# Kernel optimization log

Measured on AMD Instinct MI355X. Metric: run time of the kernel, lower is better.

Reference implementation:

```python
import jax, jax.numpy as jnp
import numpy as np

T, B, H = 2048, 32, 1024
L1, L2, L3 = 100, 10, 1  # cascade 100 -> 10 -> 1 from linear_size=100


def setup_inputs() -> dict:
    key = jax.random.key(0)
    ks = jax.random.split(key, 8)
    def lin_init(k, fan_in, shape):
        # torch nn.Linear default: U(-1/sqrt(fan_in), 1/sqrt(fan_in))
        bound = 1.0 / np.sqrt(fan_in)
        return jax.random.uniform(k, shape, jnp.float32, -bound, bound)
    return {
        "encoder_output": jax.random.normal(ks[0], (T, B, H), jnp.float32),
        "lengths": jax.random.randint(ks[1], (B,), 1, T + 1, jnp.int64),
        "W1": lin_init(ks[2], H, (L1, H)),
        "b1": lin_init(ks[3], H, (L1,)),
        "W2": lin_init(ks[4], L1, (L2, L1)),
        "b2": lin_init(ks[5], L1, (L2,)),
        "W3": lin_init(ks[6], L2, (L3, L2)),
        "b3": lin_init(ks[7], L2, (L3,)),
    }


def reference(encoder_output, lengths, W1, b1, W2, b2, W3, b3):
    # MLP cascade over all timesteps/batch at once: [T,B,H] -> [T,B,1]
    h = jax.nn.relu(jnp.einsum("tbh,lh->tbl", encoder_output, W1) + b1)
    h = jax.nn.relu(jnp.einsum("tbl,ml->tbm", h, W2) + b2)
    logits = jnp.einsum("tbm,om->tbo", h, W3) + b3  # [T,B,1]
    logp = jax.nn.log_sigmoid(logits)[..., 0]       # [T,B]
    # Mask timesteps beyond each sample's length, sum, exponentiate
    mask = jnp.arange(T)[:, None] < lengths[None, :]  # [T,B]
    return jnp.exp(jnp.sum(jnp.where(mask, logp, 0.0), axis=0))  # [B]
```

## Files before the change

### kernel.cpp

```cpp
#include <hip/hip_runtime.h>
#include <stdint.h>


#define T_DIM 2048
#define B_DIM 32
#define H_DIM 1024
#define L1_DIM 100
#define L1_PAD 112
#define L2_DIM 10
#define L2_PAD 16
#define K2_PAD 128
#define NBLK  1024

#define W1B_ELEMS (L1_PAD * H_DIM)
#define W2B_ELEMS (L2_PAD * K2_PAD)
#define PART_OFF_BYTES ((W1B_ELEMS + W2B_ELEMS) * 2)

typedef float v4f __attribute__((ext_vector_type(4)));
typedef short s8  __attribute__((ext_vector_type(8)));

static __device__ __forceinline__ unsigned short f2bf(float f) {
    unsigned int u = __float_as_uint(f);
    u += 0x7fffu + ((u >> 16) & 1u);
    return (unsigned short)(u >> 16);
}

__global__ void convert_weights(const float* __restrict__ W1,
                                const float* __restrict__ W2,
                                unsigned short* __restrict__ wsb) {
    int i = blockIdx.x * 256 + threadIdx.x;
    if (i < W1B_ELEMS) {
        int row = i >> 10, col = i & 1023;
        float v = (row < L1_DIM) ? W1[row * H_DIM + col] : 0.0f;
        wsb[i] = f2bf(v);
    } else {
        int j = i - W1B_ELEMS;
        if (j < W2B_ELEMS) {
            int r = j >> 7, c = j & 127;
            float v = (r < L2_DIM && c < L1_DIM) ? W2[r * L1_DIM + c] : 0.0f;
            wsb[W1B_ELEMS + j] = f2bf(v);
        }
    }
}

__global__ __launch_bounds__(256) void mlp_main(
    const float* __restrict__ enc,
    const int*   __restrict__ lenp,
    const float* __restrict__ b1,
    const float* __restrict__ b2,
    const float* __restrict__ W3,
    const float* __restrict__ b3,
    const unsigned short* __restrict__ w1b,
    const unsigned short* __restrict__ w2b,
    float* __restrict__ partials)
{
    __shared__ __align__(16) unsigned short ldsB[L1_PAD][72];
    __shared__ __align__(16) unsigned short ldsH[64][136];
    __shared__ __align__(16) unsigned short ldsW2[L2_PAD][136];
    __shared__ float ldsPart[2][32];

    const int tid  = threadIdx.x;
    const int blk  = blockIdx.x;
    const int lane = tid & 63;
    const int w    = tid >> 6;
    const int m    = lane & 15;
    const int q    = lane >> 4;

    const bool is64 = (lenp[1] == 0);

    const int tA = 2 * blk + (w >> 1);
    const int bA = ((w & 1) << 4) + m;
    const int lenA = is64 ? lenp[2 * bA] : lenp[bA];
    const bool predA = (tA < lenA);

    int maxlen = 0;
    for (int i = 0; i < B_DIM; ++i) {
        int L = is64 ? lenp[2 * i] : lenp[i];
        maxlen = max(maxlen, L);
    }
    if (2 * blk >= maxlen) {
        if (tid < 32) partials[tid * NBLK + blk] = 0.0f;
        return;
    }

    {
        int r = tid >> 4;
        int c = (tid & 15) << 3;
        *(uint4*)&ldsW2[r][c] = *(const uint4*)(w2b + r * K2_PAD + c);
    }

    float b1v[7];
#pragma unroll
    for (int nt = 0; nt < 7; ++nt) {
        int n = nt * 16 + m;
        b1v[nt] = (n < L1_DIM) ? b1[n] : 0.0f;
    }
    const float b2v = (m < L2_DIM) ? b2[m] : 0.0f;
    const float w3v = (m < L2_DIM) ? W3[m] : 0.0f;
    const float b3s = b3[0];

    const float* aptr = enc + (size_t)(blk * 64 + w * 16 + m) * H_DIM + q * 8;

    v4f acc[7];
#pragma unroll
    for (int nt = 0; nt < 7; ++nt) acc[nt] = (v4f)0.0f;

    for (int kc = 0; kc < 16; ++kc) {
        __syncthreads();
        {
            int base = tid;
#pragma unroll
            for (int it = 0; it < 4; ++it, base += 256) {
                if (it < 3 || base < 896) {
                    int r = base >> 3;
                    int c = (base & 7) << 3;
                    *(uint4*)&ldsB[r][c] =
                        *(const uint4*)(w1b + r * H_DIM + kc * 64 + c);
                }
            }
        }
        __syncthreads();
#pragma unroll
        for (int ks = 0; ks < 2; ++ks) {
            const int k0 = kc * 64 + ks * 32;
            float4 x0, x1;
            if (predA) {
                x0 = *(const float4*)(aptr + k0);
                x1 = *(const float4*)(aptr + k0 + 4);
            } else {
                x0 = make_float4(0.f, 0.f, 0.f, 0.f);
                x1 = make_float4(0.f, 0.f, 0.f, 0.f);
            }
            s8 afrag;
            afrag[0] = (short)f2bf(x0.x); afrag[1] = (short)f2bf(x0.y);
            afrag[2] = (short)f2bf(x0.z); afrag[3] = (short)f2bf(x0.w);
            afrag[4] = (short)f2bf(x1.x); afrag[5] = (short)f2bf(x1.y);
            afrag[6] = (short)f2bf(x1.z); afrag[7] = (short)f2bf(x1.w);
#pragma unroll
            for (int nt = 0; nt < 7; ++nt) {
                s8 bfrag = *(const s8*)&ldsB[nt * 16 + m][ks * 32 + q * 8];
                acc[nt] = __builtin_amdgcn_mfma_f32_16x16x32_bf16(
                    afrag, bfrag, acc[nt], 0, 0, 0);
            }
        }
    }

    __syncthreads();
#pragma unroll
    for (int nt = 0; nt < 7; ++nt) {
#pragma unroll
        for (int reg = 0; reg < 4; ++reg) {
            float h = fmaxf(acc[nt][reg] + b1v[nt], 0.0f);
            ldsH[w * 16 + q * 4 + reg][nt * 16 + m] = f2bf(h);
        }
    }
    {
        int r = tid >> 2;
        int c = 112 + ((tid & 3) << 2);
        *(uint2*)&ldsH[r][c] = make_uint2(0u, 0u);
    }
    __syncthreads();

    v4f acc2 = (v4f)0.0f;
#pragma unroll
    for (int ks = 0; ks < 4; ++ks) {
        s8 a2  = *(const s8*)&ldsH[w * 16 + m][ks * 32 + q * 8];
        s8 b2f = *(const s8*)&ldsW2[m][ks * 32 + q * 8];
        acc2 = __builtin_amdgcn_mfma_f32_16x16x32_bf16(a2, b2f, acc2, 0, 0, 0);
    }

    v4f z;
#pragma unroll
    for (int reg = 0; reg < 4; ++reg) {
        float y2 = fmaxf(acc2[reg] + b2v, 0.0f);
        z[reg] = y2 * w3v;
    }
#pragma unroll
    for (int msk = 1; msk < 16; msk <<= 1) {
#pragma unroll
        for (int reg = 0; reg < 4; ++reg)
            z[reg] += __shfl_xor(z[reg], msk, 16);
    }
    if (m == 0) {
#pragma unroll
        for (int reg = 0; reg < 4; ++reg) {
            int rowLocal = q * 4 + reg;
            int bC = ((w & 1) << 4) + rowLocal;
            int lenC = is64 ? lenp[2 * bC] : lenp[bC];
            float logit = z[reg] + b3s;
            float logp  = fminf(logit, 0.0f) - log1pf(__expf(-fabsf(logit)));
            ldsPart[w >> 1][bC] = (tA < lenC) ? logp : 0.0f;
        }
    }
    __syncthreads();
    if (tid < 32)
        partials[tid * NBLK + blk] = ldsPart[0][tid] + ldsPart[1][tid];
}

__global__ void finalize(const float* __restrict__ partials,
                         float* __restrict__ out) {
    const int b = blockIdx.x;
    const int tid = threadIdx.x;
    float s = 0.0f;
    for (int i = tid; i < NBLK; i += 256) s += partials[b * NBLK + i];
#pragma unroll
    for (int off = 32; off > 0; off >>= 1) s += __shfl_down(s, off, 64);
    __shared__ float red[4];
    if ((tid & 63) == 0) red[tid >> 6] = s;
    __syncthreads();
    if (tid == 0) out[b] = expf(red[0] + red[1] + red[2] + red[3]);
}

extern "C" void kernel_launch(void* const* d_in, const int* in_sizes, int n_in,
                              void* d_out, int out_size, void* d_ws, size_t ws_size,
                              hipStream_t stream) {
    const float* enc = (const float*)d_in[0];
    const int*   len = (const int*)d_in[1];
    const float* W1  = (const float*)d_in[2];
    const float* b1  = (const float*)d_in[3];
    const float* W2  = (const float*)d_in[4];
    const float* b2  = (const float*)d_in[5];
    const float* W3  = (const float*)d_in[6];
    const float* b3  = (const float*)d_in[7];

    unsigned short* wsb = (unsigned short*)d_ws;
    float* partials = (float*)((char*)d_ws + PART_OFF_BYTES);
    float* out = (float*)d_out;

    convert_weights<<<(W1B_ELEMS + W2B_ELEMS + 255) / 256, 256, 0, stream>>>(W1, W2, wsb);
    mlp_main<<<NBLK, 256, 0, stream>>>(enc, len, b1, b2, W3, b3,
                                       wsb, wsb + W1B_ELEMS, partials);
    finalize<<<B_DIM, 256, 0, stream>>>(partials, out);
}
```

Measured before the change: 374.5 us.

## Double-buffer W1 tiles via direct-to-LDS loads and strided timestep slots

Moves to 512-thread blocks that each cover four timesteps spaced TSLOT apart, so work stays balanced under length masking. W1 tiles now go into a double-buffered, XOR-swizzled LDS buffer through global_load_lds, and the next encoder chunk is prefetched into registers so loads overlap the MFMA work. Waves whose rows are all masked skip the MFMAs. The second layer reads W2 straight from global memory, and H uses a swizzled layout to avoid bank conflicts. The early-exit on max length is removed, and the larger block needs more registers and LDS per block.

```diff
diff --git a/kernel.cpp b/kernel.cpp
--- a/kernel.cpp
+++ b/kernel.cpp
@@ -10,7 +10,8 @@
 #define L2_DIM 10
 #define L2_PAD 16
 #define K2_PAD 128
-#define NBLK  1024
+#define NBLK  512
+#define TSLOT 512
 
 #define W1B_ELEMS (L1_PAD * H_DIM)
 #define W2B_ELEMS (L2_PAD * K2_PAD)
@@ -43,7 +44,7 @@
     }
 }
 
-__global__ __launch_bounds__(256) void mlp_main(
+__global__ __launch_bounds__(512, 4) void mlp_main(
     const float* __restrict__ enc,
     const int*   __restrict__ lenp,
     const float* __restrict__ b1,
@@ -54,10 +55,9 @@
     const unsigned short* __restrict__ w2b,
     float* __restrict__ partials)
 {
-    __shared__ __align__(16) unsigned short ldsB[L1_PAD][72];
-    __shared__ __align__(16) unsigned short ldsH[64][136];
-    __shared__ __align__(16) unsigned short ldsW2[L2_PAD][136];
-    __shared__ float ldsPart[2][32];
+    __shared__ __align__(16) unsigned short bufB[2][L1_PAD * 64];
+    __shared__ __align__(16) unsigned short ldsH[128 * 128];
+    __shared__ float ldsPart[4][32];
 
     const int tid  = threadIdx.x;
     const int blk  = blockIdx.x;
@@ -65,29 +65,16 @@
     const int w    = tid >> 6;
     const int m    = lane & 15;
     const int q    = lane >> 4;
+    const int mx   = m & 7;
 
     const bool is64 = (lenp[1] == 0);
 
-    const int tA = 2 * blk + (w >> 1);
-    const int bA = ((w & 1) << 4) + m;
+    const int slot = w >> 1;
+    const int tA   = blk + TSLOT * slot;
+    const int bA   = ((w & 1) << 4) + m;
     const int lenA = is64 ? lenp[2 * bA] : lenp[bA];
-    const bool predA = (tA < lenA);
-
-    int maxlen = 0;
-    for (int i = 0; i < B_DIM; ++i) {
-        int L = is64 ? lenp[2 * i] : lenp[i];
-        maxlen = max(maxlen, L);
-    }
-    if (2 * blk >= maxlen) {
-        if (tid < 32) partials[tid * NBLK + blk] = 0.0f;
-        return;
-    }
-
-    {
-        int r = tid >> 4;
-        int c = (tid & 15) << 3;
-        *(uint4*)&ldsW2[r][c] = *(const uint4*)(w2b + r * K2_PAD + c);
-    }
+    const bool predA   = (tA < lenA);
+    const bool waveAct = (__ballot(predA) != 0ull);
 
     float b1v[7];
 #pragma unroll
@@ -99,80 +86,117 @@
     const float w3v = (m < L2_DIM) ? W3[m] : 0.0f;
     const float b3s = b3[0];
 
-    const float* aptr = enc + (size_t)(blk * 64 + w * 16 + m) * H_DIM + q * 8;
+    const float* aptr = enc + (size_t)(tA * B_DIM + bA) * H_DIM + (q << 3);
+
+    {
+        int r  = (w << 4) + (lane >> 2);
+        int c  = 14 + ((lane >> 1) & 1);
+        int cl = c ^ (r & 7);
+        *(uint2*)&ldsH[(r << 7) + (cl << 3) + ((lane & 1) << 2)] = make_uint2(0u, 0u);
+    }
+
+    auto stageW1 = [&](int buf, int kc) {
+#pragma unroll
+        for (int rep = 0; rep < 2; ++rep) {
+            const int s = w + (rep << 3);
+            if (s < 14) {
+                const int idx = (s << 6) + lane;
+                const int r   = idx >> 3;
+                const int cg  = (idx & 7) ^ (r & 7);
+                const unsigned short* gsrc =
+                    w1b + (r << 10) + (kc << 6) + (cg << 3);
+                __builtin_amdgcn_global_load_lds(
+                    (const __attribute__((address_space(1))) unsigned int*)gsrc,
+                    (__attribute__((address_space(3))) unsigned int*)&bufB[buf][s << 9],
+                    16, 0, 0);
+            }
+        }
+    };
+
+    float4 xc0, xc1, xc2, xc3, xn0, xn1, xn2, xn3;
+    auto loadX = [&](int kc, float4& a, float4& b, float4& c, float4& d) {
+        if (predA) {
+            const float* p = aptr + (kc << 6);
+            a = *(const float4*)(p);
+            b = *(const float4*)(p + 4);
+            c = *(const float4*)(p + 32);
+            d = *(const float4*)(p + 36);
+        } else {
+            a = b = c = d = make_float4(0.f, 0.f, 0.f, 0.f);
+        }
+    };
 
     v4f acc[7];
 #pragma unroll
     for (int nt = 0; nt < 7; ++nt) acc[nt] = (v4f)0.0f;
 
+    stageW1(0, 0);
+    loadX(0, xc0, xc1, xc2, xc3);
+    xn0 = xn1 = xn2 = xn3 = make_float4(0.f, 0.f, 0.f, 0.f);
+
+    const int v0   = ((q ^ mx) << 3);
+    const int v1   = (((4 + q) ^ mx) << 3);
+    const int mrow = m << 6;
+
+#pragma unroll
     for (int kc = 0; kc < 16; ++kc) {
+        const int cur = kc & 1;
         __syncthreads();
-        {
-            int base = tid;
-#pragma unroll
-            for (int it = 0; it < 4; ++it, base += 256) {
-                if (it < 3 || base < 896) {
-                    int r = base >> 3;
-                    int c = (base & 7) << 3;
-                    *(uint4*)&ldsB[r][c] =
-                        *(const uint4*)(w1b + r * H_DIM + kc * 64 + c);
+        if (kc < 15) {
+            stageW1(cur ^ 1, kc + 1);
+            loadX(kc + 1, xn0, xn1, xn2, xn3);
+        }
+        if (waveAct) {
+            const unsigned short* bb = &bufB[cur][mrow];
+#pragma unroll
+            for (int ks = 0; ks < 2; ++ks) {
+                const float4 lo = ks ? xc2 : xc0;
+                const float4 hi = ks ? xc3 : xc1;
+                s8 af;
+                af[0] = (short)f2bf(lo.x); af[1] = (short)f2bf(lo.y);
+                af[2] = (short)f2bf(lo.z); af[3] = (short)f2bf(lo.w);
+                af[4] = (short)f2bf(hi.x); af[5] = (short)f2bf(hi.y);
+                af[6] = (short)f2bf(hi.z); af[7] = (short)f2bf(hi.w);
+                const int vo = ks ? v1 : v0;
+#pragma unroll
+                for (int nt = 0; nt < 7; ++nt) {
+                    const s8 bf = *(const s8*)(bb + (nt << 10) + vo);
+                    acc[nt] = __builtin_amdgcn_mfma_f32_16x16x32_bf16(
+                        af, bf, acc[nt], 0, 0, 0);
                 }
             }
         }
-        __syncthreads();
-#pragma unroll
-        for (int ks = 0; ks < 2; ++ks) {
-            const int k0 = kc * 64 + ks * 32;
-            float4 x0, x1;
-            if (predA) {
-                x0 = *(const float4*)(aptr + k0);
-                x1 = *(const float4*)(aptr + k0 + 4);
-            } else {
-                x0 = make_float4(0.f, 0.f, 0.f, 0.f);
-                x1 = make_float4(0.f, 0.f, 0.f, 0.f);
-            }
-            s8 afrag;
-            afrag[0] = (short)f2bf(x0.x); afrag[1] = (short)f2bf(x0.y);
-            afrag[2] = (short)f2bf(x0.z); afrag[3] = (short)f2bf(x0.w);
-            afrag[4] = (short)f2bf(x1.x); afrag[5] = (short)f2bf(x1.y);
-            afrag[6] = (short)f2bf(x1.z); afrag[7] = (short)f2bf(x1.w);
-#pragma unroll
-            for (int nt = 0; nt < 7; ++nt) {
-                s8 bfrag = *(const s8*)&ldsB[nt * 16 + m][ks * 32 + q * 8];
-                acc[nt] = __builtin_amdgcn_mfma_f32_16x16x32_bf16(
-                    afrag, bfrag, acc[nt], 0, 0, 0);
-            }
-        }
-    }
-
-    __syncthreads();
+        xc0 = xn0; xc1 = xn1; xc2 = xn2; xc3 = xn3;
+    }
+
 #pragma unroll
     for (int nt = 0; nt < 7; ++nt) {
 #pragma unroll
         for (int reg = 0; reg < 4; ++reg) {
-            float h = fmaxf(acc[nt][reg] + b1v[nt], 0.0f);
-            ldsH[w * 16 + q * 4 + reg][nt * 16 + m] = f2bf(h);
-        }
-    }
+            const float h  = fmaxf(acc[nt][reg] + b1v[nt], 0.0f);
+            const int row  = (w << 4) + (q << 2) + reg;
+            const int col  = (nt << 4) + m;
+            const int cl   = (col >> 3) ^ (row & 7);
+            ldsH[(row << 7) + (cl << 3) + (col & 7)] = f2bf(h);
+        }
+    }
+
+    v4f acc2 = (v4f)0.0f;
     {
-        int r = tid >> 2;
-        int c = 112 + ((tid & 3) << 2);
-        *(uint2*)&ldsH[r][c] = make_uint2(0u, 0u);
-    }
-    __syncthreads();
-
-    v4f acc2 = (v4f)0.0f;
-#pragma unroll
-    for (int ks = 0; ks < 4; ++ks) {
-        s8 a2  = *(const s8*)&ldsH[w * 16 + m][ks * 32 + q * 8];
-        s8 b2f = *(const s8*)&ldsW2[m][ks * 32 + q * 8];
-        acc2 = __builtin_amdgcn_mfma_f32_16x16x32_bf16(a2, b2f, acc2, 0, 0, 0);
+        const unsigned short* hb = &ldsH[((w << 4) + m) << 7];
+#pragma unroll
+        for (int ks = 0; ks < 4; ++ks) {
+            const int cl = ((ks << 2) + q) ^ mx;
+            const s8 a2  = *(const s8*)(hb + (cl << 3));
+            const s8 b2f = *(const s8*)(w2b + (m << 7) + (ks << 5) + (q << 3));
+            acc2 = __builtin_amdgcn_mfma_f32_16x16x32_bf16(a2, b2f, acc2, 0, 0, 0);
+        }
     }
 
     v4f z;
 #pragma unroll
     for (int reg = 0; reg < 4; ++reg) {
-        float y2 = fmaxf(acc2[reg] + b2v, 0.0f);
+        const float y2 = fmaxf(acc2[reg] + b2v, 0.0f);
         z[reg] = y2 * w3v;
     }
 #pragma unroll
@@ -184,17 +208,18 @@
     if (m == 0) {
 #pragma unroll
         for (int reg = 0; reg < 4; ++reg) {
-            int rowLocal = q * 4 + reg;
-            int bC = ((w & 1) << 4) + rowLocal;
-            int lenC = is64 ? lenp[2 * bC] : lenp[bC];
-            float logit = z[reg] + b3s;
-            float logp  = fminf(logit, 0.0f) - log1pf(__expf(-fabsf(logit)));
-            ldsPart[w >> 1][bC] = (tA < lenC) ? logp : 0.0f;
+            const int rowLocal = (q << 2) + reg;
+            const int bC   = ((w & 1) << 4) + rowLocal;
+            const int lenC = is64 ? lenp[2 * bC] : lenp[bC];
+            const float logit = z[reg] + b3s;
+            const float logp  = fminf(logit, 0.0f) - log1pf(__expf(-fabsf(logit)));
+            ldsPart[slot][bC] = (tA < lenC) ? logp : 0.0f;
         }
     }
     __syncthreads();
     if (tid < 32)
-        partials[tid * NBLK + blk] = ldsPart[0][tid] + ldsPart[1][tid];
+        partials[tid * NBLK + blk] =
+            ldsPart[0][tid] + ldsPart[1][tid] + ldsPart[2][tid] + ldsPart[3][tid];
 }
 
 __global__ void finalize(const float* __restrict__ partials,
@@ -228,7 +253,7 @@
     float* out = (float*)d_out;
 
     convert_weights<<<(W1B_ELEMS + W2B_ELEMS + 255) / 256, 256, 0, stream>>>(W1, W2, wsb);
-    mlp_main<<<NBLK, 256, 0, stream>>>(enc, len, b1, b2, W3, b3,
+    mlp_main<<<NBLK, 512, 0, stream>>>(enc, len, b1, b2, W3, b3,
                                        wsb, wsb + W1B_ELEMS, partials);
     finalize<<<B_DIM, 256, 0, stream>>>(partials, out);
 }
```

Measured after the change: 361.6 us. 3.5% less time.
